# Optimization experiments

Hardware: AMD Instinct MI355X
Metric: run time of the kernel (lower is better)

Reference implementation:

```python
import jax, jax.numpy as jnp
import numpy as np

VOCAB, D, E, K = 32000, 1024, 8, 2
B, T = 2, 2048
EPS = 1e-5


def setup_inputs() -> dict:
    key = jax.random.key(0)
    ks = jax.random.split(key, 8)
    s = 0.02  # init scale
    return {
        "x": jax.random.randint(ks[0], (B, T), 0, VOCAB, dtype=jnp.int64)
        if jax.config.jax_enable_x64 else jax.random.randint(ks[0], (B, T), 0, VOCAB, dtype=jnp.int32),
        "embed_W": jax.random.normal(ks[1], (VOCAB, D), jnp.float32) * s,
        "gate_W": jax.random.normal(ks[2], (E, D), jnp.float32) * s,
        "gate_b": jnp.zeros((E,), jnp.float32),
        "W1": jax.random.normal(ks[3], (E, D, 2 * D), jnp.float32) * s,
        "b1": jnp.zeros((E, 2 * D), jnp.float32),
        "W2": jax.random.normal(ks[4], (E, 2 * D, D), jnp.float32) * s,
        "b2": jnp.zeros((E, D), jnp.float32),
        "ln_g": jnp.ones((D,), jnp.float32),
        "ln_b": jnp.zeros((D,), jnp.float32),
        "head_W": jax.random.normal(ks[5], (VOCAB, D), jnp.float32) * s,
        "head_b": jnp.zeros((VOCAB,), jnp.float32),
    }


def reference(x, embed_W, gate_W, gate_b, W1, b1, W2, b2, ln_g, ln_b, head_W, head_b):
    # --- forward_pre: embed + router softmax + top-k ---
    h = embed_W[x]                                   # [B,T,D]
    gate_logits = h @ gate_W.T + gate_b              # [B,T,E]
    probs = jax.nn.softmax(gate_logits, axis=-1)
    topk_vals, topk_idx = jax.lax.top_k(probs, K)    # [B,T,K]

    N = B * T
    hf = h.reshape(N, D)
    tv = topk_vals.reshape(N, K)
    ti = topk_idx.reshape(N, K)

    # --- per-expert MLP (dense over experts; combine with sparse gates) ---
    a = jax.nn.relu(jnp.einsum('nd,edh->enh', hf, W1) + b1[:, None, :])   # [E,N,2D]
    eo = jnp.einsum('enh,ehd->end', a, W2) + b2[:, None, :]               # [E,N,D]

    gates = jnp.zeros((N, E), hf.dtype).at[jnp.arange(N)[:, None], ti].set(tv)
    y = jnp.einsum('end,ne->nd', eo, gates)          # [N,D] combined output

    # --- forward_post: LayerNorm + vocab head ---
    mu = jnp.mean(y, axis=-1, keepdims=True)
    var = jnp.var(y, axis=-1, keepdims=True)
    yn = (y - mu) * jax.lax.rsqrt(var + EPS) * ln_g + ln_b
    logits = yn @ head_W.T + head_b                  # [B*T, VOCAB]
    return logits, topk_idx
```

## Files before the change

### kernel.cpp

```cpp
#include <hip/hip_runtime.h>

typedef short bf16x8 __attribute__((ext_vector_type(8)));
typedef float f32x4 __attribute__((ext_vector_type(4)));
typedef unsigned short u16;

#define NT 4096
#define DM 1024
#define DF 2048
#define NE 8
#define NV 32000

__device__ __forceinline__ u16 f2bf(float f) {
  unsigned u = __float_as_uint(f);
  u += 0x7fffu + ((u >> 16) & 1u);
  return (u16)(u >> 16);
}

__device__ __forceinline__ void async16(const void* g, void* l) {
  __builtin_amdgcn_global_load_lds(
      (const __attribute__((address_space(1))) void*)g,
      (__attribute__((address_space(3))) void*)l, 16, 0, 0);
}

__global__ void cvt_bf16_kernel(const float* __restrict__ src, u16* __restrict__ dst, int n4) {
  int i = blockIdx.x * blockDim.x + threadIdx.x;
  int stride = gridDim.x * blockDim.x;
  for (; i < n4; i += stride) {
    float4 v = ((const float4*)src)[i];
    ushort4 o;
    o.x = f2bf(v.x); o.y = f2bf(v.y); o.z = f2bf(v.z); o.w = f2bf(v.w);
    ((ushort4*)dst)[i] = o;
  }
}

__global__ void transpose_cvt_kernel(const float* __restrict__ W, u16* __restrict__ WT, int R, int C) {
  __shared__ float tile[32][33];
  int e = blockIdx.z;
  const float* We = W + (size_t)e * R * C;
  u16* WTe = WT + (size_t)e * R * C;
  int c0 = blockIdx.x * 32, r0 = blockIdx.y * 32;
  int tx = threadIdx.x, ty = threadIdx.y;
  #pragma unroll
  for (int i = 0; i < 32; i += 8)
    tile[ty + i][tx] = We[(size_t)(r0 + ty + i) * C + (c0 + tx)];
  __syncthreads();
  #pragma unroll
  for (int i = 0; i < 32; i += 8)
    WTe[(size_t)(c0 + ty + i) * R + (r0 + tx)] = f2bf(tile[tx][ty + i]);
}

__global__ void embed_gate_kernel(const int* __restrict__ x, const float* __restrict__ embW,
                                  const float* __restrict__ gateW, const float* __restrict__ gateb,
                                  u16* __restrict__ A1, int* __restrict__ dest, float* __restrict__ gatev,
                                  int* __restrict__ cnt, float* __restrict__ topk_out) {
  int n = blockIdx.x, tid = threadIdx.x;
  int row = x[n];
  float4 h4 = ((const float4*)(embW + (size_t)row * DM))[tid];
  float p[NE];
  #pragma unroll
  for (int e = 0; e < NE; ++e) {
    float4 w = ((const float4*)(gateW + e * DM))[tid];
    p[e] = h4.x * w.x + h4.y * w.y + h4.z * w.z + h4.w * w.w;
  }
  #pragma unroll
  for (int off = 32; off > 0; off >>= 1)
    #pragma unroll
    for (int e = 0; e < NE; ++e) p[e] += __shfl_down(p[e], off);

  __shared__ float part[4][NE];
  __shared__ int bc[4];
  int wave = tid >> 6, lane = tid & 63;
  if (lane == 0)
    for (int e = 0; e < NE; ++e) part[wave][e] = p[e];
  __syncthreads();
  if (tid == 0) {
    float l[NE];
    #pragma unroll
    for (int e = 0; e < NE; ++e)
      l[e] = part[0][e] + part[1][e] + part[2][e] + part[3][e] + gateb[e];
    float mx = l[0];
    #pragma unroll
    for (int e = 1; e < NE; ++e) mx = fmaxf(mx, l[e]);
    float pe[NE], s = 0.f;
    #pragma unroll
    for (int e = 0; e < NE; ++e) { pe[e] = expf(l[e] - mx); s += pe[e]; }
    int i1 = 0; float b1v = l[0];
    #pragma unroll
    for (int e = 1; e < NE; ++e) if (l[e] > b1v) { b1v = l[e]; i1 = e; }
    int i2 = -1; float b2v = -1e30f;
    #pragma unroll
    for (int e = 0; e < NE; ++e) if (e != i1 && l[e] > b2v) { b2v = l[e]; i2 = e; }
    float inv = 1.0f / s;
    int s1 = atomicAdd(&cnt[i1], 1);
    int s2 = atomicAdd(&cnt[i2], 1);
    dest[i1 * NT + s1] = n * 2;
    dest[i2 * NT + s2] = n * 2 + 1;
    gatev[i1 * NT + s1] = pe[i1] * inv;
    gatev[i2 * NT + s2] = pe[i2] * inv;
    topk_out[n * 2]     = (float)i1;
    topk_out[n * 2 + 1] = (float)i2;
    bc[0] = i1; bc[1] = s1; bc[2] = i2; bc[3] = s2;
  }
  __syncthreads();
  int e1 = bc[0], s1 = bc[1], e2 = bc[2], s2 = bc[3];
  ushort4 hb;
  hb.x = f2bf(h4.x); hb.y = f2bf(h4.y); hb.z = f2bf(h4.z); hb.w = f2bf(h4.w);
  ((ushort4*)(A1 + ((size_t)e1 * NT + s1) * DM))[tid] = hb;
  ((ushort4*)(A1 + ((size_t)e2 * NT + s2) * DM))[tid] = hb;
}

template <int K>
__device__ __forceinline__ void gemm_tile(const u16* __restrict__ A, const u16* __restrict__ B,
                                          f32x4 acc[4][4], u16* sA, u16* sB) {
  const int tid = threadIdx.x;
  const u16* gA = A + (size_t)(tid >> 3) * K + (tid & 7) * 8;
  const u16* gB = B + (size_t)(tid >> 3) * K + (tid & 7) * 8;
  u16* dA = sA + tid * 8;
  u16* dB = sB + tid * 8;
  const int lane = tid & 63;
  const int wm = ((tid >> 7) & 1) * 64;
  const int wn = ((tid >> 6) & 1) * 64;
  const int fm = lane & 15;
  const int fq = lane >> 4;
  const int aoff = (wm + fm) * 64 + fq * 8;
  const int boff = (wn + fm) * 64 + fq * 8;

  for (int k0 = 0; k0 < K; k0 += 64) {
    #pragma unroll
    for (int it = 0; it < 4; ++it) {
      async16(gA + (size_t)it * 32 * K + k0, dA + it * 2048);
      async16(gB + (size_t)it * 32 * K + k0, dB + it * 2048);
    }
    __syncthreads();
    #pragma unroll
    for (int ks = 0; ks < 2; ++ks) {
      bf16x8 af[4], bfr[4];
      #pragma unroll
      for (int mt = 0; mt < 4; ++mt)
        af[mt] = *(const bf16x8*)(sA + aoff + mt * 16 * 64 + ks * 32);
      #pragma unroll
      for (int nt = 0; nt < 4; ++nt)
        bfr[nt] = *(const bf16x8*)(sB + boff + nt * 16 * 64 + ks * 32);
      #pragma unroll
      for (int mt = 0; mt < 4; ++mt)
        #pragma unroll
        for (int nt = 0; nt < 4; ++nt)
          acc[mt][nt] = __builtin_amdgcn_mfma_f32_16x16x32_bf16(af[mt], bfr[nt], acc[mt][nt], 0, 0, 0);
    }
    __syncthreads();
  }
}

#define ACC_INIT(acc)                          \
  f32x4 acc[4][4];                             \
  _Pragma("unroll")                            \
  for (int i = 0; i < 4; ++i)                  \
    _Pragma("unroll")                          \
    for (int j = 0; j < 4; ++j) acc[i][j] = (f32x4){0.f, 0.f, 0.f, 0.f};

__global__ __launch_bounds__(256) void gemm1_kernel(const u16* __restrict__ A1, const u16* __restrict__ W1T,
                                                    const float* __restrict__ b1, u16* __restrict__ apack,
                                                    const int* __restrict__ cnt) {
  int e = blockIdx.z;
  int m0 = blockIdx.y * 128, n0 = blockIdx.x * 128;
  if (m0 >= cnt[e]) return;
  __shared__ u16 sA[128 * 64], sB[128 * 64];
  ACC_INIT(acc)
  gemm_tile<DM>(A1 + ((size_t)e * NT + m0) * DM, W1T + ((size_t)e * DF + n0) * DM, acc, sA, sB);
  int tid = threadIdx.x, lane = tid & 63;
  int wm = ((tid >> 7) & 1) * 64, wn = ((tid >> 6) & 1) * 64;
  int fm = lane & 15, fq = lane >> 4;
  #pragma unroll
  for (int mt = 0; mt < 4; ++mt)
    #pragma unroll
    for (int nt = 0; nt < 4; ++nt) {
      int col = n0 + wn + nt * 16 + fm;
      float bias = b1[e * DF + col];
      #pragma unroll
      for (int r = 0; r < 4; ++r) {
        int m = m0 + wm + mt * 16 + fq * 4 + r;
        apack[((size_t)e * NT + m) * DF + col] = f2bf(fmaxf(acc[mt][nt][r] + bias, 0.f));
      }
    }
}

__global__ __launch_bounds__(256) void gemm2_kernel(const u16* __restrict__ apack, const u16* __restrict__ W2T,
                                                    const float* __restrict__ b2, const int* __restrict__ dest,
                                                    const float* __restrict__ gatev, const int* __restrict__ cnt,
                                                    float* __restrict__ ypair) {
  int e = blockIdx.z;
  int m0 = blockIdx.y * 128, n0 = blockIdx.x * 128;
  int ce = cnt[e];
  if (m0 >= ce) return;
  __shared__ u16 sA[128 * 64], sB[128 * 64];
  ACC_INIT(acc)
  gemm_tile<DF>(apack + ((size_t)e * NT + m0) * DF, W2T + ((size_t)e * DM + n0) * DF, acc, sA, sB);
  int tid = threadIdx.x, lane = tid & 63;
  int wm = ((tid >> 7) & 1) * 64, wn = ((tid >> 6) & 1) * 64;
  int fm = lane & 15, fq = lane >> 4;
  #pragma unroll
  for (int mt = 0; mt < 4; ++mt)
    #pragma unroll
    for (int r = 0; r < 4; ++r) {
      int m = m0 + wm + mt * 16 + fq * 4 + r;
      if (m < ce) {
        int d = dest[e * NT + m];
        float gv = gatev[e * NT + m];
        #pragma unroll
        for (int nt = 0; nt < 4; ++nt) {
          int col = n0 + wn + nt * 16 + fm;
          ypair[(size_t)d * DM + col] = gv * (acc[mt][nt][r] + b2[e * DM + col]);
        }
      }
    }
}

__global__ void combine_ln_kernel(const float* __restrict__ ypair, const float* __restrict__ g,
                                  const float* __restrict__ b, u16* __restrict__ yn) {
  int n = blockIdx.x, tid = threadIdx.x;
  float4 va = ((const float4*)(ypair + (size_t)(2 * n) * DM))[tid];
  float4 vb = ((const float4*)(ypair + (size_t)(2 * n + 1) * DM))[tid];
  float4 v;
  v.x = va.x + vb.x; v.y = va.y + vb.y; v.z = va.z + vb.z; v.w = va.w + vb.w;
  float s = v.x + v.y + v.z + v.w;
  float q = v.x * v.x + v.y * v.y + v.z * v.z + v.w * v.w;
  #pragma unroll
  for (int off = 32; off > 0; off >>= 1) {
    s += __shfl_down(s, off);
    q += __shfl_down(q, off);
  }
  __shared__ float red[4][2];
  __shared__ float mr[2];
  int wave = tid >> 6, lane = tid & 63;
  if (lane == 0) { red[wave][0] = s; red[wave][1] = q; }
  __syncthreads();
  if (tid == 0) {
    float S = red[0][0] + red[1][0] + red[2][0] + red[3][0];
    float Q = red[0][1] + red[1][1] + red[2][1] + red[3][1];
    float mu = S * (1.0f / DM);
    float var = Q * (1.0f / DM) - mu * mu;
    mr[0] = mu;
    mr[1] = rsqrtf(var + 1e-5f);
  }
  __syncthreads();
  float mu = mr[0], r = mr[1];
  float4 gg = ((const float4*)g)[tid];
  float4 bb = ((const float4*)b)[tid];
  ushort4 o;
  o.x = f2bf((v.x - mu) * r * gg.x + bb.x);
  o.y = f2bf((v.y - mu) * r * gg.y + bb.y);
  o.z = f2bf((v.z - mu) * r * gg.z + bb.z);
  o.w = f2bf((v.w - mu) * r * gg.w + bb.w);
  ((ushort4*)(yn + (size_t)n * DM))[tid] = o;
}

__global__ __launch_bounds__(256) void head_kernel(const u16* __restrict__ yn, const u16* __restrict__ hw,
                                                   const float* __restrict__ hb, float* __restrict__ out) {
  int m0 = blockIdx.x * 128, n0 = blockIdx.y * 128;
  __shared__ u16 sA[128 * 64], sB[128 * 64];
  ACC_INIT(acc)
  gemm_tile<DM>(yn + (size_t)m0 * DM, hw + (size_t)n0 * DM, acc, sA, sB);
  int tid = threadIdx.x, lane = tid & 63;
  int wm = ((tid >> 7) & 1) * 64, wn = ((tid >> 6) & 1) * 64;
  int fm = lane & 15, fq = lane >> 4;
  #pragma unroll
  for (int mt = 0; mt < 4; ++mt)
    #pragma unroll
    for (int nt = 0; nt < 4; ++nt) {
      int col = n0 + wn + nt * 16 + fm;
      float bias = hb[col];
      #pragma unroll
      for (int r = 0; r < 4; ++r) {
        int m = m0 + wm + mt * 16 + fq * 4 + r;
        out[(size_t)m * NV + col] = acc[mt][nt][r] + bias;
      }
    }
}

extern "C" void kernel_launch(void* const* d_in, const int* in_sizes, int n_in,
                              void* d_out, int out_size, void* d_ws, size_t ws_size,
                              hipStream_t stream) {
  const int*   x     = (const int*)  d_in[0];
  const float* embW  = (const float*)d_in[1];
  const float* gateW = (const float*)d_in[2];
  const float* gateb = (const float*)d_in[3];
  const float* W1    = (const float*)d_in[4];
  const float* b1    = (const float*)d_in[5];
  const float* W2    = (const float*)d_in[6];
  const float* b2    = (const float*)d_in[7];
  const float* lng   = (const float*)d_in[8];
  const float* lnb   = (const float*)d_in[9];
  const float* headW = (const float*)d_in[10];
  const float* headb = (const float*)d_in[11];
  float* out = (float*)d_out;

  char* ob = (char*)d_out;
  u16*   A1    = (u16*)  (ob + 0);
  u16*   APACK = (u16*)  (ob + 67108864);
  float* YPAIR = (float*)(ob + 201326592);
  u16*   W1T   = (u16*)  (ob + 234881024);
  u16*   W2T   = (u16*)  (ob + 268435456);
  float* TOPK  = (float*)(ob + 524288000);

  char* wb = (char*)d_ws;
  u16*   HWB  = (u16*)  (wb);
  u16*   YN   = (u16*)  (wb + 65536000);
  int*   DEST = (int*)  (wb + 73924608);
  float* GV   = (float*)(wb + 74055680);
  int*   CNT  = (int*)  (wb + 74186752);

  hipMemsetAsync(CNT, 0, NE * sizeof(int), stream);
  cvt_bf16_kernel<<<4096, 256, 0, stream>>>(headW, HWB, NV * DM / 4);
  transpose_cvt_kernel<<<dim3(DF / 32, DM / 32, NE), dim3(32, 8), 0, stream>>>(W1, W1T, DM, DF);
  transpose_cvt_kernel<<<dim3(DM / 32, DF / 32, NE), dim3(32, 8), 0, stream>>>(W2, W2T, DF, DM);
  embed_gate_kernel<<<NT, 256, 0, stream>>>(x, embW, gateW, gateb, A1, DEST, GV, CNT, TOPK);
  gemm1_kernel<<<dim3(DF / 128, NT / 128, NE), 256, 0, stream>>>(A1, W1T, b1, APACK, CNT);
  gemm2_kernel<<<dim3(DM / 128, NT / 128, NE), 256, 0, stream>>>(APACK, W2T, b2, DEST, GV, CNT, YPAIR);
  combine_ln_kernel<<<NT, 256, 0, stream>>>(YPAIR, lng, lnb, YN);
  head_kernel<<<dim3(NT / 128, NV / 128), 256, 0, stream>>>(YN, HWB, headb, out);
}
```

Measured before the change: 1.439 ms.

## Rewrite vocab head GEMM with 256x256 tiles, double-buffered async loads, XCD swizzle

The head GEMM moves from 128x128 tiles on 256 threads to 256x256 tiles on 512 threads (8 waves, each computing 128x64). Global-to-LDS async loads are double-buffered so the next K slice is fetched while MFMAs run on the current one. Block indices are remapped by XCD so neighbouring tiles share L2 and operand data is reused more. The larger tiles need 128 KB of LDS and many accumulator registers, which limits occupancy, and the grid drops to 2000 blocks.

```diff
diff --git a/kernel.cpp b/kernel.cpp
--- a/kernel.cpp
+++ b/kernel.cpp
@@ -254,17 +254,85 @@
   ((ushort4*)(yn + (size_t)n * DM))[tid] = o;
 }
 
-__global__ __launch_bounds__(256) void head_kernel(const u16* __restrict__ yn, const u16* __restrict__ hw,
-                                                   const float* __restrict__ hb, float* __restrict__ out) {
-  int m0 = blockIdx.x * 128, n0 = blockIdx.y * 128;
-  __shared__ u16 sA[128 * 64], sB[128 * 64];
-  ACC_INIT(acc)
-  gemm_tile<DM>(yn + (size_t)m0 * DM, hw + (size_t)n0 * DM, acc, sA, sB);
-  int tid = threadIdx.x, lane = tid & 63;
-  int wm = ((tid >> 7) & 1) * 64, wn = ((tid >> 6) & 1) * 64;
-  int fm = lane & 15, fq = lane >> 4;
-  #pragma unroll
-  for (int mt = 0; mt < 4; ++mt)
+__global__ __launch_bounds__(512, 2) void head_kernel(const u16* __restrict__ yn, const u16* __restrict__ hw,
+                                                      const float* __restrict__ hb, float* __restrict__ out) {
+  int flat = blockIdx.y * gridDim.x + blockIdx.x;
+  int xcd = flat & 7, pos = flat >> 3;
+  int swz = xcd * 250 + pos;
+  int m0 = (swz & 15) * 256;
+  int n0 = (swz >> 4) * 256;
+
+  __shared__ u16 sA0[256 * 64], sB0[256 * 64], sA1[256 * 64], sB1[256 * 64];
+
+  const int tid = threadIdx.x;
+  const int lane = tid & 63;
+  const int wid = tid >> 6;
+  const int wm = (wid >> 2) * 128;
+  const int wn = (wid & 3) * 64;
+  const int fm = lane & 15;
+  const int fq = lane >> 4;
+
+  const u16* gA = yn + (size_t)(m0 + (tid >> 3)) * DM + (tid & 7) * 8;
+  const u16* gB = hw + (size_t)(n0 + (tid >> 3)) * DM + (tid & 7) * 8;
+  const int ldst = tid * 8;
+
+  f32x4 acc[8][4];
+  #pragma unroll
+  for (int i = 0; i < 8; ++i)
+    #pragma unroll
+    for (int j = 0; j < 4; ++j) acc[i][j] = (f32x4){0.f, 0.f, 0.f, 0.f};
+
+  u16 *pa = sA0, *pb = sB0, *qa = sA1, *qb = sB1;
+
+  #pragma unroll
+  for (int i = 0; i < 4; ++i) {
+    async16(gA + (size_t)i * 64 * DM, pa + i * 4096 + ldst);
+    async16(gB + (size_t)i * 64 * DM, pb + i * 4096 + ldst);
+  }
+
+  const int NK = DM / 64;
+  for (int t = 0; t < NK; ++t) {
+    if (t < NK - 1) {
+      int k0 = (t + 1) * 64;
+      #pragma unroll
+      for (int i = 0; i < 4; ++i) {
+        async16(gA + (size_t)i * 64 * DM + k0, qa + i * 4096 + ldst);
+        async16(gB + (size_t)i * 64 * DM + k0, qb + i * 4096 + ldst);
+      }
+      asm volatile("s_waitcnt vmcnt(8)" ::: "memory");
+    } else {
+      asm volatile("s_waitcnt vmcnt(0)" ::: "memory");
+    }
+    __builtin_amdgcn_sched_barrier(0);
+    __builtin_amdgcn_s_barrier();
+    __builtin_amdgcn_sched_barrier(0);
+
+    #pragma unroll
+    for (int ks = 0; ks < 2; ++ks) {
+      bf16x8 bfr[4];
+      #pragma unroll
+      for (int nt = 0; nt < 4; ++nt)
+        bfr[nt] = *(const bf16x8*)(pb + (wn + nt * 16 + fm) * 64 + ks * 32 + fq * 8);
+      #pragma unroll
+      for (int mt = 0; mt < 8; ++mt) {
+        bf16x8 af = *(const bf16x8*)(pa + (wm + mt * 16 + fm) * 64 + ks * 32 + fq * 8);
+        #pragma unroll
+        for (int nt = 0; nt < 4; ++nt)
+          acc[mt][nt] = __builtin_amdgcn_mfma_f32_16x16x32_bf16(af, bfr[nt], acc[mt][nt], 0, 0, 0);
+      }
+    }
+
+    __builtin_amdgcn_sched_barrier(0);
+    __builtin_amdgcn_s_barrier();
+    __builtin_amdgcn_sched_barrier(0);
+
+    u16* tmp;
+    tmp = pa; pa = qa; qa = tmp;
+    tmp = pb; pb = qb; qb = tmp;
+  }
+
+  #pragma unroll
+  for (int mt = 0; mt < 8; ++mt)
     #pragma unroll
     for (int nt = 0; nt < 4; ++nt) {
       int col = n0 + wn + nt * 16 + fm;
@@ -317,5 +385,5 @@
   gemm1_kernel<<<dim3(DF / 128, NT / 128, NE), 256, 0, stream>>>(A1, W1T, b1, APACK, CNT);
   gemm2_kernel<<<dim3(DM / 128, NT / 128, NE), 256, 0, stream>>>(APACK, W2T, b2, DEST, GV, CNT, YPAIR);
   combine_ln_kernel<<<NT, 256, 0, stream>>>(YPAIR, lng, lnb, YN);
-  head_kernel<<<dim3(NT / 128, NV / 128), 256, 0, stream>>>(YN, HWB, headb, out);
-}
+  head_kernel<<<dim3(16, 125), 512, 0, stream>>>(YN, HWB, headb, out);
+}
```

Measured after the change: 1.428 ms. Within noise of the previous version (-0.7%).
